# Optimization experiments

Measured on AMD Instinct MI355X. Metric: run time of the kernel, lower is better.

Reference implementation:

```python
import jax, jax.numpy as jnp
import numpy as np

NUM_HEADS = 16
HEAD_DIM = 128
CHUNK = 256
ROPE_BASE = 10000.0


def rotate_half(x):
    x1 = x[..., ::2]
    x2 = x[..., 1::2]
    return jnp.stack((-x2, x1), axis=-1).reshape(x.shape)


def rope_cos_sin(seq_len, head_dim):
    inv_freq = 1.0 / (ROPE_BASE ** (np.arange(0, head_dim, 2, dtype=np.float32) / head_dim))
    pos = np.arange(seq_len, dtype=np.float32)
    freqs = np.outer(pos, inv_freq)                  # [S, D/2]
    emb = np.concatenate([freqs, freqs], axis=-1)    # [S, D]
    return jnp.asarray(np.cos(emb)), jnp.asarray(np.sin(emb))


def setup_inputs() -> dict:
    key = jax.random.key(0)
    k1, k2, k3 = jax.random.split(key, 3)
    B, S, E = 2, 4096, 2048
    x = jax.random.normal(k1, (B, S, E), dtype=jnp.float32)
    W_qkv = jax.random.normal(k2, (3 * E, E), dtype=jnp.float32) * 0.02
    W_out = jax.random.normal(k3, (E, E), dtype=jnp.float32) * 0.02
    return {"x": x, "W_qkv": W_qkv, "W_out": W_out}


def reference(x, W_qkv, W_out):
    B, S, E = x.shape
    H, D = NUM_HEADS, HEAD_DIM
    qkv = x @ W_qkv.T                                  # [B,S,3E]
    qkv = qkv.reshape(B, S, 3, H, D).transpose(2, 0, 3, 1, 4)  # [3,B,H,S,D]
    q, k, v = qkv[0], qkv[1], qkv[2]

    cos, sin = rope_cos_sin(S, D)                      # [S,D]
    cos = cos[None, None]
    sin = sin[None, None]
    q = q * cos + rotate_half(q) * sin
    k = k * cos + rotate_half(k) * sin

    # ELU+1 feature map
    q = jax.nn.elu(q) + 1.0
    k = jax.nn.elu(k) + 1.0

    n_chunks = S // CHUNK
    # [n,B,H,C,D]
    to_chunks = lambda t: t.reshape(B, H, n_chunks, CHUNK, D).transpose(2, 0, 1, 3, 4)
    qs, ks, vs = to_chunks(q), to_chunks(k), to_chunks(v)

    tril = jnp.tril(jnp.ones((CHUNK, CHUNK), dtype=x.dtype))  # inclusive causal mask

    def step(carry, qkv_c):
        S_c, Z_c = carry
        qc, kc, vc = qkv_c
        att = jnp.einsum('bhld,bhmd->bhlm', qc, kc) * tril       # intra-chunk causal scores
        num = jnp.einsum('bhlm,bhme->bhle', att, vc) + jnp.einsum('bhld,bhde->bhle', qc, S_c)
        den = att.sum(-1) + jnp.einsum('bhld,bhd->bhl', qc, Z_c)
        S_new = S_c + jnp.einsum('bhld,bhle->bhde', kc, vc)
        Z_new = Z_c + kc.sum(axis=2)
        return (S_new, Z_new), (num, den)

    S0 = jnp.zeros((B, H, D, D), dtype=x.dtype)
    Z0 = jnp.zeros((B, H, D), dtype=x.dtype)
    _, (num, den) = jax.lax.scan(step, (S0, Z0), (qs, ks, vs))
    # num: [n,B,H,C,D] -> [B,H,S,D]; den: [n,B,H,C] -> [B,H,S]
    num = num.transpose(1, 2, 0, 3, 4).reshape(B, H, S, D)
    den = den.transpose(1, 2, 0, 3).reshape(B, H, S)
    den = jnp.maximum(den, 1e-6)

    out = num / den[..., None]                          # [B,H,S,D]
    out = out.transpose(0, 2, 1, 3).reshape(B, S, H * D)
    return out @ W_out.T
```

## Files before the change

### kernel.cpp

```cpp
#include <hip/hip_runtime.h>
#include <cmath>

#define Ss 4096
#define NCh 16
#define CK 256

typedef unsigned short bfu;
typedef __bf16 bf16x8 __attribute__((ext_vector_type(8)));
typedef float f32x4 __attribute__((ext_vector_type(4)));
typedef unsigned short u16x8 __attribute__((ext_vector_type(8)));

__device__ __forceinline__ float bf2f(unsigned short u) {
    union { unsigned u32; float f; } v; v.u32 = ((unsigned)u) << 16; return v.f;
}
__device__ __forceinline__ unsigned short f2bf(float f) {
    union { float f; unsigned u; } v; v.f = f;
    unsigned r = v.u + 0x7fff + ((v.u >> 16) & 1);
    return (unsigned short)(r >> 16);
}

__device__ __forceinline__ void g2l16(void* lds, const void* g) {
    __builtin_amdgcn_global_load_lds(
        (const __attribute__((address_space(1))) void*)g,
        (__attribute__((address_space(3))) void*)lds, 16, 0, 0);
}

__global__ void rope_table(float* __restrict__ cosT, float* __restrict__ sinT) {
    int id = blockIdx.x * 256 + threadIdx.x;
    int f = id & 63, s = id >> 6;
    float e = (2.0f * (float)f) / 128.0f;
    float inv = 1.0f / powf(10000.0f, e);
    float ang = (float)s * inv;
    cosT[id] = cosf(ang);
    sinT[id] = sinf(ang);
}

__global__ void conv_bf16(const float* __restrict__ in, bfu* __restrict__ out, int n4) {
    for (int i = blockIdx.x * 256 + threadIdx.x; i < n4; i += gridDim.x * 256) {
        float4 v = ((const float4*)in)[i];
        ushort4 o;
        o.x = f2bf(v.x); o.y = f2bf(v.y); o.z = f2bf(v.z); o.w = f2bf(v.w);
        ((ushort4*)out)[i] = o;
    }
}

template<int EPI>
__global__ __launch_bounds__(512) void gemm8p(
    const bfu* __restrict__ A, const bfu* __restrict__ B,
    const float* __restrict__ cosT, const float* __restrict__ sinT,
    bfu* __restrict__ qb, bfu* __restrict__ kb,
    bfu* __restrict__ kT, bfu* __restrict__ vT,
    float* __restrict__ outF)
{
    __shared__ bfu AsL[3 * 256 * 64];
    __shared__ bfu BsL[3 * 128 * 64];
    const int tid = threadIdx.x;
    const int wid = tid >> 6, lane = tid & 63;
    const int wm = wid >> 2, wn = wid & 3;
    const int bm = blockIdx.y * 256, bn = blockIdx.x * 128;
    const int l15 = lane & 15, l7 = lane & 7, lhi = lane >> 4;

    const int arow = (wm * 128 + l15) * 128;
    const int brow = (wn * 32 + l15) * 128;
    const int sl0 = ((lhi + 0) ^ l7) * 16;
    const int sl1 = ((lhi + 4) ^ l7) * 16;

    const int rl = tid >> 3;
    const int scol = ((tid & 7) ^ (rl & 7)) * 8;
    const bfu* Ab = A + (size_t)(bm + rl) * 2048 + scol;
    const bfu* Bb = B + (size_t)(bn + rl) * 2048 + scol;
    bfu* AsW = AsL + wid * 512;
    bfu* BsW = BsL + wid * 512;

    f32x4 acc[8][2] = {};

    auto stage = [&](int T, int sbuf, int h) {
        const size_t kofs = (size_t)T * 64;
        if (h == 0) {
            g2l16(AsW + sbuf * 16384 + 0 * 4096, Ab + kofs);
            g2l16(AsW + sbuf * 16384 + 1 * 4096, Ab + kofs + 131072);
            g2l16(BsW + sbuf * 8192  + 0 * 4096, Bb + kofs);
        } else {
            g2l16(AsW + sbuf * 16384 + 2 * 4096, Ab + kofs + 262144);
            g2l16(AsW + sbuf * 16384 + 3 * 4096, Ab + kofs + 393216);
            g2l16(BsW + sbuf * 8192  + 1 * 4096, Bb + kofs + 131072);
        }
    };

    stage(0, 0, 0); stage(0, 0, 1);
    stage(1, 1, 0); stage(1, 1, 1);
    asm volatile("s_waitcnt vmcnt(6)" ::: "memory");
    __builtin_amdgcn_s_barrier();
    asm volatile("" ::: "memory");

    for (int T = 0; T < 32; ++T) {
        const int buf = T % 3;
        const int sbuf = (T + 2) % 3;
        const bool doStage = (T < 30);
        const char* Abl = (const char*)AsL + buf * 32768;
        const char* Bbl = (const char*)BsL + buf * 16384;

        bf16x8 af0[4][2], bfrg[2][2];
#pragma unroll
        for (int mi = 0; mi < 4; ++mi) {
            af0[mi][0] = *(const bf16x8*)(Abl + arow + mi * 2048 + sl0);
            af0[mi][1] = *(const bf16x8*)(Abl + arow + mi * 2048 + sl1);
        }
#pragma unroll
        for (int ni = 0; ni < 2; ++ni) {
            bfrg[ni][0] = *(const bf16x8*)(Bbl + brow + ni * 2048 + sl0);
            bfrg[ni][1] = *(const bf16x8*)(Bbl + brow + ni * 2048 + sl1);
        }
        if (doStage) stage(T + 2, sbuf, 0);
        __builtin_amdgcn_s_barrier();
        asm volatile("s_waitcnt lgkmcnt(0)" ::: "memory");
        __builtin_amdgcn_sched_barrier(0);
        __builtin_amdgcn_s_setprio(1);
#pragma unroll
        for (int mi = 0; mi < 4; ++mi)
#pragma unroll
            for (int ni = 0; ni < 2; ++ni) {
                acc[mi][ni] = __builtin_amdgcn_mfma_f32_16x16x32_bf16(af0[mi][0], bfrg[ni][0], acc[mi][ni], 0, 0, 0);
                acc[mi][ni] = __builtin_amdgcn_mfma_f32_16x16x32_bf16(af0[mi][1], bfrg[ni][1], acc[mi][ni], 0, 0, 0);
            }
        __builtin_amdgcn_s_setprio(0);
        __builtin_amdgcn_s_barrier();
        asm volatile("" ::: "memory");

        bf16x8 af1[4][2];
#pragma unroll
        for (int mi = 0; mi < 4; ++mi) {
            af1[mi][0] = *(const bf16x8*)(Abl + arow + (mi + 4) * 2048 + sl0);
            af1[mi][1] = *(const bf16x8*)(Abl + arow + (mi + 4) * 2048 + sl1);
        }
        if (doStage) stage(T + 2, sbuf, 1);
        __builtin_amdgcn_s_barrier();
        asm volatile("s_waitcnt lgkmcnt(0)" ::: "memory");
        __builtin_amdgcn_sched_barrier(0);
        __builtin_amdgcn_s_setprio(1);
#pragma unroll
        for (int mi = 0; mi < 4; ++mi)
#pragma unroll
            for (int ni = 0; ni < 2; ++ni) {
                acc[mi + 4][ni] = __builtin_amdgcn_mfma_f32_16x16x32_bf16(af1[mi][0], bfrg[ni][0], acc[mi + 4][ni], 0, 0, 0);
                acc[mi + 4][ni] = __builtin_amdgcn_mfma_f32_16x16x32_bf16(af1[mi][1], bfrg[ni][1], acc[mi + 4][ni], 0, 0, 0);
            }
        __builtin_amdgcn_s_setprio(0);
        if (T < 30) { asm volatile("s_waitcnt vmcnt(6)" ::: "memory"); }
        else        { asm volatile("s_waitcnt vmcnt(0)" ::: "memory"); }
        __builtin_amdgcn_s_barrier();
        asm volatile("" ::: "memory");
    }

    if constexpr (EPI == 0) {
        const int part = bn >> 11;
        const int headcol = bn & 2047;
        const int head = headcol >> 7;
#pragma unroll
        for (int mi = 0; mi < 8; ++mi) {
            const int m0 = bm + wm * 128 + mi * 16 + (lhi << 2);
            const int bq = m0 >> 12;
            const int sloc = m0 & 4095;
#pragma unroll
            for (int ni = 0; ni < 2; ++ni) {
                const int d = wn * 32 + ni * 16 + l15;
                const int f = d & 63;
                float vv[4];
#pragma unroll
                for (int r = 0; r < 4; ++r) {
                    float v = acc[mi][ni][r];
                    float p = __shfl_xor(v, 1);
                    if (part < 2) {
                        const int s = (m0 + r) & 4095;
                        float cc = cosT[s * 64 + f], sn = sinT[s * 64 + f];
                        float o = (d & 1) ? v * cc + p * sn : v * cc - p * sn;
                        v = o > 0.0f ? o + 1.0f : __expf(o);
                    }
                    vv[r] = v;
                }
                if (part == 0) {
#pragma unroll
                    for (int r = 0; r < 4; ++r)
                        qb[(size_t)(m0 + r) * 2048 + headcol + d] = f2bf(vv[r]);
                } else if (part == 1) {
#pragma unroll
                    for (int r = 0; r < 4; ++r)
                        kb[(size_t)(m0 + r) * 2048 + headcol + d] = f2bf(vv[r]);
                    ushort4 t4;
                    t4.x = f2bf(vv[0]); t4.y = f2bf(vv[1]); t4.z = f2bf(vv[2]); t4.w = f2bf(vv[3]);
                    *(ushort4*)(kT + ((size_t)(bq * 16 + head) * 128 + d) * 4096 + sloc) = t4;
                } else {
                    ushort4 t4;
                    t4.x = f2bf(vv[0]); t4.y = f2bf(vv[1]); t4.z = f2bf(vv[2]); t4.w = f2bf(vv[3]);
                    *(ushort4*)(vT + ((size_t)(bq * 16 + head) * 128 + d) * 4096 + sloc) = t4;
                }
            }
        }
    } else {
#pragma unroll
        for (int mi = 0; mi < 8; ++mi) {
            const int m0 = bm + wm * 128 + mi * 16 + (lhi << 2);
#pragma unroll
            for (int ni = 0; ni < 2; ++ni) {
                const int n = bn + wn * 32 + ni * 16 + l15;
#pragma unroll
                for (int r = 0; r < 4; ++r)
                    outF[(size_t)(m0 + r) * 2048 + n] = acc[mi][ni][r];
            }
        }
    }
}

__global__ __launch_bounds__(256) void kv_outer_mfma(
    const bfu* __restrict__ vT, const bfu* __restrict__ kT,
    bfu* __restrict__ Scb, float* __restrict__ Zc)
{
    __shared__ bfu As[128 * 64];
    __shared__ bfu Bs[128 * 64];
    __shared__ float zS[128][2];
    const int batch = blockIdx.x;
    const int c = batch & 15, h = (batch >> 4) & 15, b = batch >> 8;
    const size_t fbase = (size_t)(b * 16 + h) * 128 * 4096 + c * 256;
    const int tid = threadIdx.x, wid = tid >> 6, lane = tid & 63;
    const int wr = wid >> 1, wc = wid & 1;
    const int srow = lane >> 3, scol = (lane & 7) * 8;
    f32x4 acc[4][4] = {};
    float zreg = 0.0f;
    const int zd = tid >> 1, zo = (tid & 1) * 32;

    for (int k0 = 0; k0 < 256; k0 += 64) {
        __syncthreads();
#pragma unroll
        for (int i = 0; i < 4; ++i) {
            const int r = i * 32 + wid * 8;
            g2l16(&As[r * 64], vT + fbase + (size_t)(r + srow) * 4096 + k0 + scol);
            g2l16(&Bs[r * 64], kT + fbase + (size_t)(r + srow) * 4096 + k0 + scol);
        }
        __syncthreads();
#pragma unroll
        for (int ks = 0; ks < 2; ++ks) {
            bf16x8 af[4], bfr[4];
#pragma unroll
            for (int mi = 0; mi < 4; ++mi)
                af[mi] = *(const bf16x8*)&As[(wr * 64 + mi * 16 + (lane & 15)) * 64 + ks * 32 + (lane >> 4) * 8];
#pragma unroll
            for (int ni = 0; ni < 4; ++ni)
                bfr[ni] = *(const bf16x8*)&Bs[(wc * 64 + ni * 16 + (lane & 15)) * 64 + ks * 32 + (lane >> 4) * 8];
#pragma unroll
            for (int mi = 0; mi < 4; ++mi)
#pragma unroll
                for (int ni = 0; ni < 4; ++ni)
                    acc[mi][ni] = __builtin_amdgcn_mfma_f32_16x16x32_bf16(af[mi], bfr[ni], acc[mi][ni], 0, 0, 0);
        }
#pragma unroll
        for (int j = 0; j < 32; ++j) zreg += bf2f(Bs[zd * 64 + zo + j]);
    }
    zS[zd][tid & 1] = zreg;
    __syncthreads();
    if (tid < 128) Zc[(size_t)batch * 128 + tid] = zS[tid][0] + zS[tid][1];
    bfu* Sout = Scb + (size_t)batch * 16384;
#pragma unroll
    for (int mi = 0; mi < 4; ++mi)
#pragma unroll
        for (int ni = 0; ni < 4; ++ni) {
            const int d = wc * 64 + ni * 16 + (lane & 15);
#pragma unroll
            for (int r = 0; r < 4; ++r) {
                const int e = wr * 64 + mi * 16 + ((lane >> 4) << 2) + r;
                Sout[e * 128 + d] = f2bf(acc[mi][ni][r]);
            }
        }
}

__global__ void prefix_Sb(bfu* __restrict__ Scb) {
    size_t idx = (size_t)blockIdx.x * 256 + threadIdx.x;
    size_t bh = idx >> 14, de = idx & 16383;
    bfu* p = Scb + bh * (size_t)NCh * 16384 + de;
    float run = 0.0f;
#pragma unroll
    for (int c = 0; c < NCh; ++c) {
        float t = bf2f(p[(size_t)c * 16384]);
        p[(size_t)c * 16384] = f2bf(run);
        run += t;
    }
}
__global__ void prefix_Z(float* __restrict__ Zc) {
    size_t idx = (size_t)blockIdx.x * 256 + threadIdx.x;
    size_t bh = idx >> 7, d = idx & 127;
    float* p = Zc + bh * (size_t)NCh * 128 + d;
    float run = 0.0f;
#pragma unroll
    for (int c = 0; c < NCh; ++c) {
        float t = p[(size_t)c * 128];
        p[(size_t)c * 128] = run;
        run += t;
    }
}

__global__ __launch_bounds__(256) void chunk_mfma(
    const bfu* __restrict__ qb, const bfu* __restrict__ kb,
    const bfu* __restrict__ vT, const bfu* __restrict__ Scb,
    const float* __restrict__ Zc, bfu* __restrict__ ao)
{
    __shared__ bfu shrd[16384];
    __shared__ bfu attL[16384];
    __shared__ float Zs[128];
    __shared__ float denS[128][2];
    const int half = blockIdx.x, batch = blockIdx.y;
    const int c = batch & 15, h = (batch >> 4) & 15, b = batch >> 8;
    const int row0 = b * Ss + c * CK;
    const int tid = threadIdx.x, wid = tid >> 6, lane = tid & 63;
    const int wr = wid >> 1, wc = wid & 1;
    const int sr = lane >> 4, sc8 = (lane & 15) * 8;
    if (tid < 128) Zs[tid] = Zc[(size_t)batch * 128 + tid];

    bf16x8 qf[4][4];
    {
        const bfu* qrow = qb + (size_t)(row0 + half * 128 + wr * 64 + (lane & 15)) * 2048
                          + h * 128 + (lane >> 4) * 8;
#pragma unroll
        for (int mi = 0; mi < 4; ++mi)
#pragma unroll
            for (int ks = 0; ks < 4; ++ks)
                qf[mi][ks] = *(const bf16x8*)(qrow + (size_t)mi * 16 * 2048 + ks * 32);
    }
    f32x4 num[4][4] = {};
    float den_reg = 0.0f;
    const int dl = tid >> 1, dc0 = (tid & 1) * 64;

    for (int kb_ = 0; kb_ <= half; ++kb_) {
        __syncthreads();
#pragma unroll
        for (int i = 0; i < 8; ++i) {
            const int r = i * 16 + wid * 4;
            g2l16(&shrd[r * 128], kb + (size_t)(row0 + kb_ * 128 + r + sr) * 2048 + h * 128 + sc8);
        }
        __syncthreads();
        f32x4 attacc[4][4] = {};
#pragma unroll
        for (int ks = 0; ks < 4; ++ks) {
            bf16x8 bfr[4];
#pragma unroll
            for (int ni = 0; ni < 4; ++ni)
                bfr[ni] = *(const bf16x8*)&shrd[(wc * 64 + ni * 16 + (lane & 15)) * 128 + ks * 32 + (lane >> 4) * 8];
#pragma unroll
            for (int mi = 0; mi < 4; ++mi)
#pragma unroll
                for (int ni = 0; ni < 4; ++ni)
                    attacc[mi][ni] = __builtin_amdgcn_mfma_f32_16x16x32_bf16(qf[mi][ks], bfr[ni], attacc[mi][ni], 0, 0, 0);
        }
        __syncthreads();
#pragma unroll
        for (int i = 0; i < 8; ++i) {
            const int r = i * 16 + wid * 4;
            g2l16(&shrd[r * 128],
                  vT + ((size_t)(b * 16 + h) * 128 + r + sr) * 4096 + c * 256 + kb_ * 128 + sc8);
        }
        const bool needmask = (kb_ == half);
#pragma unroll
        for (int mi = 0; mi < 4; ++mi)
#pragma unroll
            for (int ni = 0; ni < 4; ++ni) {
                const int l0 = wr * 64 + mi * 16 + ((lane >> 4) << 2);
                const int m = wc * 64 + ni * 16 + (lane & 15);
#pragma unroll
                for (int r = 0; r < 4; ++r) {
                    const int l = l0 + r;
                    float v = attacc[mi][ni][r];
                    if (needmask && (half * 128 + l) < (kb_ * 128 + m)) v = 0.0f;
                    const int byte = (l * 256 + m * 2) ^ ((l & 7) << 4);
                    *(bfu*)((char*)attL + byte) = f2bf(v);
                }
            }
        __syncthreads();
#pragma unroll
        for (int ks = 0; ks < 4; ++ks) {
            bf16x8 af[4], bfr[4];
#pragma unroll
            for (int mi = 0; mi < 4; ++mi) {
                const int l = wr * 64 + mi * 16 + (lane & 15);
                const int byte = (l * 256 + (ks * 32 + (lane >> 4) * 8) * 2) ^ ((l & 7) << 4);
                af[mi] = *(const bf16x8*)((const char*)attL + byte);
            }
#pragma unroll
            for (int ni = 0; ni < 4; ++ni)
                bfr[ni] = *(const bf16x8*)&shrd[(wc * 64 + ni * 16 + (lane & 15)) * 128 + ks * 32 + (lane >> 4) * 8];
#pragma unroll
            for (int mi = 0; mi < 4; ++mi)
#pragma unroll
                for (int ni = 0; ni < 4; ++ni)
                    num[mi][ni] = __builtin_amdgcn_mfma_f32_16x16x32_bf16(af[mi], bfr[ni], num[mi][ni], 0, 0, 0);
        }
#pragma unroll
        for (int j8 = 0; j8 < 8; ++j8) {
            const int byte = (dl * 256 + (dc0 + j8 * 8) * 2) ^ ((dl & 7) << 4);
            u16x8 a = *(const u16x8*)((const char*)attL + byte);
#pragma unroll
            for (int jj = 0; jj < 8; ++jj) den_reg += bf2f(a[jj]);
        }
    }
    __syncthreads();
#pragma unroll
    for (int i = 0; i < 8; ++i) {
        const int r = i * 16 + wid * 4;
        g2l16(&shrd[r * 128], Scb + (size_t)batch * 16384 + (size_t)(r + sr) * 128 + sc8);
    }
    __syncthreads();
#pragma unroll
    for (int ks = 0; ks < 4; ++ks) {
        bf16x8 bfr[4];
#pragma unroll
        for (int ni = 0; ni < 4; ++ni)
            bfr[ni] = *(const bf16x8*)&shrd[(wc * 64 + ni * 16 + (lane & 15)) * 128 + ks * 32 + (lane >> 4) * 8];
#pragma unroll
        for (int mi = 0; mi < 4; ++mi)
#pragma unroll
            for (int ni = 0; ni < 4; ++ni)
                num[mi][ni] = __builtin_amdgcn_mfma_f32_16x16x32_bf16(qf[mi][ks], bfr[ni], num[mi][ni], 0, 0, 0);
    }
    {
        const bfu* qrow = qb + (size_t)(row0 + half * 128 + dl) * 2048 + h * 128 + dc0;
#pragma unroll
        for (int j8 = 0; j8 < 8; ++j8) {
            u16x8 a = *(const u16x8*)(qrow + j8 * 8);
#pragma unroll
            for (int jj = 0; jj < 8; ++jj) den_reg += bf2f(a[jj]) * Zs[dc0 + j8 * 8 + jj];
        }
    }
    denS[dl][tid & 1] = den_reg;
    __syncthreads();
    bfu* aop = ao + (size_t)(row0 + half * 128) * 2048 + h * 128;
#pragma unroll
    for (int mi = 0; mi < 4; ++mi)
#pragma unroll
        for (int ni = 0; ni < 4; ++ni) {
            const int e = wc * 64 + ni * 16 + (lane & 15);
#pragma unroll
            for (int r = 0; r < 4; ++r) {
                const int l = wr * 64 + mi * 16 + ((lane >> 4) << 2) + r;
                float dv = denS[l][0] + denS[l][1];
                dv = dv > 1e-6f ? dv : 1e-6f;
                aop[(size_t)l * 2048 + e] = f2bf(num[mi][ni][r] / dv);
            }
        }
}

extern "C" void kernel_launch(void* const* d_in, const int* in_sizes, int n_in,
                              void* d_out, int out_size, void* d_ws, size_t ws_size,
                              hipStream_t stream)
{
    const float* x    = (const float*)d_in[0];
    const float* Wqkv = (const float*)d_in[1];
    const float* Wout = (const float*)d_in[2];
    float* out = (float*)d_out;
    char* ws = (char*)d_ws;

    bfu* xb   = (bfu*)(ws);
    bfu* ao   = (bfu*)(ws);
    bfu* wqb  = (bfu*)(ws + 33554432);
    bfu* wob  = (bfu*)(ws + 33554432);
    float* cosT = (float*)(ws + 58720256);
    float* sinT = (float*)(ws + 59768832);
    bfu* Scb  = (bfu*)(ws + 60817408);
    float* Zc = (float*)(ws + 77594624);
    bfu* qb   = (bfu*)(ws + 77856768);
    bfu* kb   = (bfu*)(ws + 111411200);
    bfu* kTb  = (bfu*)(ws + 144965632);
    bfu* vTb  = (bfu*)(ws + 178520064);

    rope_table<<<1024, 256, 0, stream>>>(cosT, sinT);
    conv_bf16<<<2048, 256, 0, stream>>>(x,    xb,  4194304);
    conv_bf16<<<2048, 256, 0, stream>>>(Wqkv, wqb, 3145728);
    gemm8p<0><<<dim3(48, 32), 512, 0, stream>>>(xb, wqb, cosT, sinT, qb, kb, kTb, vTb, nullptr);
    conv_bf16<<<1024, 256, 0, stream>>>(Wout, wob, 1048576);
    kv_outer_mfma<<<512, 256, 0, stream>>>(vTb, kTb, Scb, Zc);
    prefix_Z<<<16, 256, 0, stream>>>(Zc);
    prefix_Sb<<<2048, 256, 0, stream>>>(Scb);
    chunk_mfma<<<dim3(2, 512), 256, 0, stream>>>(qb, kb, vTb, Scb, Zc, ao);
    gemm8p<1><<<dim3(16, 32), 512, 0, stream>>>(ao, wob, nullptr, nullptr, nullptr, nullptr, nullptr, nullptr, out);
}
```

Measured before the change: 513.1 us.

## Enlarge GEMM tiles to 256x256 with double-buffered staging and XCD block swizzle

The bf16 GEMM kernel grows its output tile from 256x128 to 256x256 per workgroup, so each wave now holds an 8x4 accumulator grid. Operand staging drops from triple to double buffering, with A and B loads issued separately and interleaved between four MFMA phases. A 1D grid with a modulo-8 block swizzle replaces the 2D grid, meant to spread neighbouring tiles across chiplets and improve L2 reuse. The goal is higher arithmetic intensity per LDS and global load, at the cost of more registers, fewer workgroups (256 for the output projection), and less prefetch depth.

New measurement: 471.3 us. 1.09x faster.

```diff
diff --git a/kernel.cpp b/kernel.cpp
--- a/kernel.cpp
+++ b/kernel.cpp
@@ -24,6 +24,8 @@
         (const __attribute__((address_space(1))) void*)g,
         (__attribute__((address_space(3))) void*)lds, 16, 0, 0);
 }
+
+#define MFMA __builtin_amdgcn_mfma_f32_16x16x32_bf16
 
 __global__ void rope_table(float* __restrict__ cosT, float* __restrict__ sinT) {
     int id = blockIdx.x * 256 + threadIdx.x;
@@ -45,74 +47,70 @@
 }
 
 template<int EPI>
-__global__ __launch_bounds__(512) void gemm8p(
-    const bfu* __restrict__ A, const bfu* __restrict__ B,
+__global__ __launch_bounds__(512) void gemm256(
+    const bfu* __restrict__ A, const bfu* __restrict__ B, int nbx,
     const float* __restrict__ cosT, const float* __restrict__ sinT,
     bfu* __restrict__ qb, bfu* __restrict__ kb,
     bfu* __restrict__ kT, bfu* __restrict__ vT,
     float* __restrict__ outF)
 {
-    __shared__ bfu AsL[3 * 256 * 64];
-    __shared__ bfu BsL[3 * 128 * 64];
+    __shared__ bfu AsL[2 * 256 * 64];
+    __shared__ bfu BsL[2 * 256 * 64];
+    const int nwg = gridDim.x;
+    const int q8 = nwg >> 3;
+    const int swz = (blockIdx.x & 7) * q8 + (blockIdx.x >> 3);
+    const int bm = (swz / nbx) * 256, bn = (swz % nbx) * 256;
+
     const int tid = threadIdx.x;
     const int wid = tid >> 6, lane = tid & 63;
     const int wm = wid >> 2, wn = wid & 3;
-    const int bm = blockIdx.y * 256, bn = blockIdx.x * 128;
     const int l15 = lane & 15, l7 = lane & 7, lhi = lane >> 4;
-
-    const int arow = (wm * 128 + l15) * 128;
-    const int brow = (wn * 32 + l15) * 128;
-    const int sl0 = ((lhi + 0) ^ l7) * 16;
-    const int sl1 = ((lhi + 4) ^ l7) * 16;
 
     const int rl = tid >> 3;
     const int scol = ((tid & 7) ^ (rl & 7)) * 8;
     const bfu* Ab = A + (size_t)(bm + rl) * 2048 + scol;
     const bfu* Bb = B + (size_t)(bn + rl) * 2048 + scol;
-    bfu* AsW = AsL + wid * 512;
-    bfu* BsW = BsL + wid * 512;
-
-    f32x4 acc[8][2] = {};
-
-    auto stage = [&](int T, int sbuf, int h) {
-        const size_t kofs = (size_t)T * 64;
-        if (h == 0) {
-            g2l16(AsW + sbuf * 16384 + 0 * 4096, Ab + kofs);
-            g2l16(AsW + sbuf * 16384 + 1 * 4096, Ab + kofs + 131072);
-            g2l16(BsW + sbuf * 8192  + 0 * 4096, Bb + kofs);
-        } else {
-            g2l16(AsW + sbuf * 16384 + 2 * 4096, Ab + kofs + 262144);
-            g2l16(AsW + sbuf * 16384 + 3 * 4096, Ab + kofs + 393216);
-            g2l16(BsW + sbuf * 8192  + 1 * 4096, Bb + kofs + 131072);
-        }
+
+    f32x4 acc[8][4] = {};
+
+    auto stageA = [&](int T) {
+        bfu* d = AsL + (T & 1) * 16384 + wid * 512;
+        const bfu* s = Ab + (size_t)T * 64;
+        g2l16(d,         s);
+        g2l16(d + 4096,  s + (size_t)64 * 2048);
+        g2l16(d + 8192,  s + (size_t)128 * 2048);
+        g2l16(d + 12288, s + (size_t)192 * 2048);
     };
-
-    stage(0, 0, 0); stage(0, 0, 1);
-    stage(1, 1, 0); stage(1, 1, 1);
-    asm volatile("s_waitcnt vmcnt(6)" ::: "memory");
+    auto stageB = [&](int T) {
+        bfu* d = BsL + (T & 1) * 16384 + wid * 512;
+        const bfu* s = Bb + (size_t)T * 64;
+        g2l16(d,         s);
+        g2l16(d + 4096,  s + (size_t)64 * 2048);
+        g2l16(d + 8192,  s + (size_t)128 * 2048);
+        g2l16(d + 12288, s + (size_t)192 * 2048);
+    };
+
+    stageA(0); stageB(0);
+    stageA(1); stageB(1);
+    asm volatile("s_waitcnt vmcnt(8)" ::: "memory");
     __builtin_amdgcn_s_barrier();
     asm volatile("" ::: "memory");
 
     for (int T = 0; T < 32; ++T) {
-        const int buf = T % 3;
-        const int sbuf = (T + 2) % 3;
-        const bool doStage = (T < 30);
-        const char* Abl = (const char*)AsL + buf * 32768;
-        const char* Bbl = (const char*)BsL + buf * 16384;
-
-        bf16x8 af0[4][2], bfrg[2][2];
-#pragma unroll
-        for (int mi = 0; mi < 4; ++mi) {
-            af0[mi][0] = *(const bf16x8*)(Abl + arow + mi * 2048 + sl0);
-            af0[mi][1] = *(const bf16x8*)(Abl + arow + mi * 2048 + sl1);
-        }
-#pragma unroll
-        for (int ni = 0; ni < 2; ++ni) {
-            bfrg[ni][0] = *(const bf16x8*)(Bbl + brow + ni * 2048 + sl0);
-            bfrg[ni][1] = *(const bf16x8*)(Bbl + brow + ni * 2048 + sl1);
-        }
-        if (doStage) stage(T + 2, sbuf, 0);
-        __builtin_amdgcn_s_barrier();
+        const char* Ax = (const char*)AsL + (T & 1) * 32768;
+        const char* Bx = (const char*)BsL + (T & 1) * 32768;
+        bf16x8 a0[4][2], a1[4][2], b0[2][2], b1[2][2];
+
+#pragma unroll
+        for (int mi = 0; mi < 4; ++mi)
+#pragma unroll
+            for (int ks = 0; ks < 2; ++ks)
+                a0[mi][ks] = *(const bf16x8*)(Ax + (wm * 128 + mi * 16 + l15) * 128 + (((ks * 4 + lhi) ^ l7) << 4));
+#pragma unroll
+        for (int ni = 0; ni < 2; ++ni)
+#pragma unroll
+            for (int ks = 0; ks < 2; ++ks)
+                b0[ni][ks] = *(const bf16x8*)(Bx + (wn * 64 + ni * 16 + l15) * 128 + (((ks * 4 + lhi) ^ l7) << 4));
         asm volatile("s_waitcnt lgkmcnt(0)" ::: "memory");
         __builtin_amdgcn_sched_barrier(0);
         __builtin_amdgcn_s_setprio(1);
@@ -120,21 +118,36 @@
         for (int mi = 0; mi < 4; ++mi)
 #pragma unroll
             for (int ni = 0; ni < 2; ++ni) {
-                acc[mi][ni] = __builtin_amdgcn_mfma_f32_16x16x32_bf16(af0[mi][0], bfrg[ni][0], acc[mi][ni], 0, 0, 0);
-                acc[mi][ni] = __builtin_amdgcn_mfma_f32_16x16x32_bf16(af0[mi][1], bfrg[ni][1], acc[mi][ni], 0, 0, 0);
+                acc[mi][ni] = MFMA(a0[mi][0], b0[ni][0], acc[mi][ni], 0, 0, 0);
+                acc[mi][ni] = MFMA(a0[mi][1], b0[ni][1], acc[mi][ni], 0, 0, 0);
+            }
+        __builtin_amdgcn_s_setprio(0);
+
+#pragma unroll
+        for (int ni = 0; ni < 2; ++ni)
+#pragma unroll
+            for (int ks = 0; ks < 2; ++ks)
+                b1[ni][ks] = *(const bf16x8*)(Bx + (wn * 64 + (ni + 2) * 16 + l15) * 128 + (((ks * 4 + lhi) ^ l7) << 4));
+        asm volatile("s_waitcnt lgkmcnt(0)" ::: "memory");
+        __builtin_amdgcn_sched_barrier(0);
+        __builtin_amdgcn_s_setprio(1);
+#pragma unroll
+        for (int mi = 0; mi < 4; ++mi)
+#pragma unroll
+            for (int ni = 0; ni < 2; ++ni) {
+                acc[mi][ni + 2] = MFMA(a0[mi][0], b1[ni][0], acc[mi][ni + 2], 0, 0, 0);
+                acc[mi][ni + 2] = MFMA(a0[mi][1], b1[ni][1], acc[mi][ni + 2], 0, 0, 0);
             }
         __builtin_amdgcn_s_setprio(0);
         __builtin_amdgcn_s_barrier();
         asm volatile("" ::: "memory");
 
-        bf16x8 af1[4][2];
-#pragma unroll
-        for (int mi = 0; mi < 4; ++mi) {
-            af1[mi][0] = *(const bf16x8*)(Abl + arow + (mi + 4) * 2048 + sl0);
-            af1[mi][1] = *(const bf16x8*)(Abl + arow + (mi + 4) * 2048 + sl1);
-        }
-        if (doStage) stage(T + 2, sbuf, 1);
-        __builtin_amdgcn_s_barrier();
+#pragma unroll
+        for (int mi = 0; mi < 4; ++mi)
+#pragma unroll
+            for (int ks = 0; ks < 2; ++ks)
+                a1[mi][ks] = *(const bf16x8*)(Ax + (wm * 128 + (mi + 4) * 16 + l15) * 128 + (((ks * 4 + lhi) ^ l7) << 4));
+        if (T < 30) stageB(T + 2);
         asm volatile("s_waitcnt lgkmcnt(0)" ::: "memory");
         __builtin_amdgcn_sched_barrier(0);
         __builtin_amdgcn_s_setprio(1);
@@ -142,11 +155,24 @@
         for (int mi = 0; mi < 4; ++mi)
 #pragma unroll
             for (int ni = 0; ni < 2; ++ni) {
-                acc[mi + 4][ni] = __builtin_amdgcn_mfma_f32_16x16x32_bf16(af1[mi][0], bfrg[ni][0], acc[mi + 4][ni], 0, 0, 0);
-                acc[mi + 4][ni] = __builtin_amdgcn_mfma_f32_16x16x32_bf16(af1[mi][1], bfrg[ni][1], acc[mi + 4][ni], 0, 0, 0);
+                acc[mi + 4][ni] = MFMA(a1[mi][0], b0[ni][0], acc[mi + 4][ni], 0, 0, 0);
+                acc[mi + 4][ni] = MFMA(a1[mi][1], b0[ni][1], acc[mi + 4][ni], 0, 0, 0);
             }
         __builtin_amdgcn_s_setprio(0);
-        if (T < 30) { asm volatile("s_waitcnt vmcnt(6)" ::: "memory"); }
+        __builtin_amdgcn_s_barrier();
+        asm volatile("" ::: "memory");
+
+        if (T < 30) stageA(T + 2);
+        __builtin_amdgcn_s_setprio(1);
+#pragma unroll
+        for (int mi = 0; mi < 4; ++mi)
+#pragma unroll
+            for (int ni = 0; ni < 2; ++ni) {
+                acc[mi + 4][ni + 2] = MFMA(a1[mi][0], b1[ni][0], acc[mi + 4][ni + 2], 0, 0, 0);
+                acc[mi + 4][ni + 2] = MFMA(a1[mi][1], b1[ni][1], acc[mi + 4][ni + 2], 0, 0, 0);
+            }
+        __builtin_amdgcn_s_setprio(0);
+        if (T < 30) { asm volatile("s_waitcnt vmcnt(8)" ::: "memory"); }
         else        { asm volatile("s_waitcnt vmcnt(0)" ::: "memory"); }
         __builtin_amdgcn_s_barrier();
         asm volatile("" ::: "memory");
@@ -154,16 +180,16 @@
 
     if constexpr (EPI == 0) {
         const int part = bn >> 11;
-        const int headcol = bn & 2047;
-        const int head = headcol >> 7;
 #pragma unroll
         for (int mi = 0; mi < 8; ++mi) {
             const int m0 = bm + wm * 128 + mi * 16 + (lhi << 2);
             const int bq = m0 >> 12;
             const int sloc = m0 & 4095;
 #pragma unroll
-            for (int ni = 0; ni < 2; ++ni) {
-                const int d = wn * 32 + ni * 16 + l15;
+            for (int ni = 0; ni < 4; ++ni) {
+                const int cp = (bn & 2047) + wn * 64 + ni * 16 + l15;
+                const int d = cp & 127;
+                const int head = cp >> 7;
                 const int f = d & 63;
                 float vv[4];
 #pragma unroll
@@ -181,11 +207,11 @@
                 if (part == 0) {
 #pragma unroll
                     for (int r = 0; r < 4; ++r)
-                        qb[(size_t)(m0 + r) * 2048 + headcol + d] = f2bf(vv[r]);
+                        qb[(size_t)(m0 + r) * 2048 + cp] = f2bf(vv[r]);
                 } else if (part == 1) {
 #pragma unroll
                     for (int r = 0; r < 4; ++r)
-                        kb[(size_t)(m0 + r) * 2048 + headcol + d] = f2bf(vv[r]);
+                        kb[(size_t)(m0 + r) * 2048 + cp] = f2bf(vv[r]);
                     ushort4 t4;
                     t4.x = f2bf(vv[0]); t4.y = f2bf(vv[1]); t4.z = f2bf(vv[2]); t4.w = f2bf(vv[3]);
                     *(ushort4*)(kT + ((size_t)(bq * 16 + head) * 128 + d) * 4096 + sloc) = t4;
@@ -201,8 +227,8 @@
         for (int mi = 0; mi < 8; ++mi) {
             const int m0 = bm + wm * 128 + mi * 16 + (lhi << 2);
 #pragma unroll
-            for (int ni = 0; ni < 2; ++ni) {
-                const int n = bn + wn * 32 + ni * 16 + l15;
+            for (int ni = 0; ni < 4; ++ni) {
+                const int n = bn + wn * 64 + ni * 16 + l15;
 #pragma unroll
                 for (int r = 0; r < 4; ++r)
                     outF[(size_t)(m0 + r) * 2048 + n] = acc[mi][ni][r];
@@ -250,7 +276,7 @@
             for (int mi = 0; mi < 4; ++mi)
 #pragma unroll
                 for (int ni = 0; ni < 4; ++ni)
-                    acc[mi][ni] = __builtin_amdgcn_mfma_f32_16x16x32_bf16(af[mi], bfr[ni], acc[mi][ni], 0, 0, 0);
+                    acc[mi][ni] = MFMA(af[mi], bfr[ni], acc[mi][ni], 0, 0, 0);
         }
 #pragma unroll
         for (int j = 0; j < 32; ++j) zreg += bf2f(Bs[zd * 64 + zo + j]);
@@ -347,7 +373,7 @@
             for (int mi = 0; mi < 4; ++mi)
 #pragma unroll
                 for (int ni = 0; ni < 4; ++ni)
-                    attacc[mi][ni] = __builtin_amdgcn_mfma_f32_16x16x32_bf16(qf[mi][ks], bfr[ni], attacc[mi][ni], 0, 0, 0);
+                    attacc[mi][ni] = MFMA(qf[mi][ks], bfr[ni], attacc[mi][ni], 0, 0, 0);
         }
         __syncthreads();
 #pragma unroll
@@ -389,7 +415,7 @@
             for (int mi = 0; mi < 4; ++mi)
 #pragma unroll
                 for (int ni = 0; ni < 4; ++ni)
-                    num[mi][ni] = __builtin_amdgcn_mfma_f32_16x16x32_bf16(af[mi], bfr[ni], num[mi][ni], 0, 0, 0);
+                    num[mi][ni] = MFMA(af[mi], bfr[ni], num[mi][ni], 0, 0, 0);
         }
 #pragma unroll
         for (int j8 = 0; j8 < 8; ++j8) {
@@ -416,7 +442,7 @@
         for (int mi = 0; mi < 4; ++mi)
 #pragma unroll
             for (int ni = 0; ni < 4; ++ni)
-                num[mi][ni] = __builtin_amdgcn_mfma_f32_16x16x32_bf16(qf[mi][ks], bfr[ni], num[mi][ni], 0, 0, 0);
+                num[mi][ni] = MFMA(qf[mi][ks], bfr[ni], num[mi][ni], 0, 0, 0);
     }
     {
         const bfu* qrow = qb + (size_t)(row0 + half * 128 + dl) * 2048 + h * 128 + dc0;
@@ -471,11 +497,11 @@
     rope_table<<<1024, 256, 0, stream>>>(cosT, sinT);
     conv_bf16<<<2048, 256, 0, stream>>>(x,    xb,  4194304);
     conv_bf16<<<2048, 256, 0, stream>>>(Wqkv, wqb, 3145728);
-    gemm8p<0><<<dim3(48, 32), 512, 0, stream>>>(xb, wqb, cosT, sinT, qb, kb, kTb, vTb, nullptr);
+    gemm256<0><<<768, 512, 0, stream>>>(xb, wqb, 24, cosT, sinT, qb, kb, kTb, vTb, nullptr);
     conv_bf16<<<1024, 256, 0, stream>>>(Wout, wob, 1048576);
     kv_outer_mfma<<<512, 256, 0, stream>>>(vTb, kTb, Scb, Zc);
     prefix_Z<<<16, 256, 0, stream>>>(Zc);
     prefix_Sb<<<2048, 256, 0, stream>>>(Scb);
     chunk_mfma<<<dim3(2, 512), 256, 0, stream>>>(qb, kb, vTb, Scb, Zc, ao);
-    gemm8p<1><<<dim3(16, 32), 512, 0, stream>>>(ao, wob, nullptr, nullptr, nullptr, nullptr, nullptr, nullptr, out);
-}
+    gemm256<1><<<256, 512, 0, stream>>>(ao, wob, 8, nullptr, nullptr, nullptr, nullptr, nullptr, nullptr, out);
+}
```
